# Optimization experiments

Measured on AMD Instinct MI355X. Metric: run time of the kernel, lower is better.

Reference implementation:

```python
import jax, jax.numpy as jnp
import numpy as np

SOFTCLAMP = 50.0
CAUSAL_BLOCK = 256      # causal_block_size (tokens per time block)
NUM_SPECIAL = 8         # num_special_tokens
SPECIAL_SEQ = 2048      # block_size_per_special (defaults to kv seq len)
ROPE_BASE = 10000.0


def setup_inputs() -> dict:
    key = jax.random.key(0)
    kq, kk, kv = jax.random.split(key, 3)
    b, h, hk, s, d = 2, 16, 4, 2048, 64
    q = jax.random.normal(kq, (b, h, s, d), dtype=jnp.float32)
    k = jax.random.normal(kk, (b, hk, s, d), dtype=jnp.float32)
    v = jax.random.normal(kv, (b, hk, s, d), dtype=jnp.float32)
    # standard 1D rotary angles: [seq, dim_head]
    inv_freq = 1.0 / (ROPE_BASE ** (jnp.arange(0, d, 2, dtype=jnp.float32) / d))
    freqs = jnp.arange(s, dtype=jnp.float32)[:, None] * inv_freq[None, :]  # [s, d/2]
    rotations = jnp.concatenate((freqs, freqs), axis=-1)                   # [s, d]
    return {"q": q, "k": k, "v": v, "rotations": rotations}


def _apply_rotations(rotations, t):
    # t: [b, h, s, d]; rotations: [s, d] (broadcast over batch/heads)
    x1, x2 = jnp.split(t, 2, axis=-1)
    rotated_half = jnp.concatenate((-x2, x1), axis=-1)
    return t * jnp.cos(rotations) + rotated_half * jnp.sin(rotations)


def _forward(q, k, v, rotations):
    b, h, i, d = q.shape
    hk, j = k.shape[1], k.shape[2]
    scale = d ** -0.5
    q = _apply_rotations(rotations[:i], q)
    k = _apply_rotations(rotations[:j], k)
    g = h // hk  # GQA groups
    qg = q.reshape(b, hk, g, i, d)
    sim = jnp.einsum('bhgid,bhjd->bhgij', qg, k) * scale
    # softclamp score mod
    sim = jnp.tanh(sim / SOFTCLAMP) * SOFTCLAMP
    # special-token mask (faithful to source: compares raw q/k indices)
    qi = jnp.arange(i)[:, None]
    kj = jnp.arange(j)[None, :]
    special_start = SPECIAL_SEQ - NUM_SPECIAL
    q_is_special = qi >= special_start
    k_is_special = kj >= special_start
    special_mask = ~(~q_is_special & k_is_special)  # non-special q cannot see special k
    # block-causal mask: allowed when query block >= key block
    causal_allow = (qi // CAUSAL_BLOCK) >= (kj // CAUSAL_BLOCK)
    allow = special_mask & causal_allow  # [i, j], broadcasts over b,h,g
    mask_value = -jnp.finfo(sim.dtype).max
    sim = jnp.where(allow, sim, mask_value)
    attn = jax.nn.softmax(sim, axis=-1)
    out = jnp.einsum('bhgij,bhjd->bhgid', attn, v)
    return out.reshape(b, h, i, d)


def reference(q, k, v, rotations):
    return _forward(q, k, v, rotations)
```

## Files before the change

kernel.cpp:

```cpp
#include <hip/hip_runtime.h>
#include <stdint.h>

typedef unsigned short u16;
typedef short s16x8 __attribute__((ext_vector_type(8)));
typedef float f32x4 __attribute__((ext_vector_type(4)));

#define SQ 2048
#define DH 64
#define BM 64
#define BN 64
#define STR 72
#define SPECIAL_START 2040
#define NBH 32
#define NKV 8
#define NQT 32
#define NITEMS (NBH * NQT)
#define ATTN_GRID 896
#define K1F  0.18033688011112043f
#define KPAF 4.9244826e-9f
#define KPBF -6.406040185576019e-5f
#define KEF  36.067376022224085f

union U8 { s16x8 v; short e[8]; };
union F4 { f32x4 v; float e[4]; };

__device__ __forceinline__ u16 f2bf(float x) {
    uint32_t u = __float_as_uint(x);
    return (u16)((u + 0x7fffu + ((u >> 16) & 1u)) >> 16);
}
__device__ __forceinline__ uint32_t pkbf(float a, float b) {
    uint32_t r;
    asm("v_cvt_pk_bf16_f32 %0, %1, %2" : "=v"(r) : "v"(a), "v"(b));
    return r;
}
__device__ __forceinline__ float exp2hw(float x) {
    float r; asm("v_exp_f32 %0, %1" : "=v"(r) : "v"(x)); return r;
}
__device__ __forceinline__ float2 fsincos(float ang) {
    float r = ang * 0.15915494309189535f;
    r -= floorf(r);
    float s, c;
    asm("v_sin_f32 %0, %1" : "=v"(s) : "v"(r));
    asm("v_cos_f32 %0, %1" : "=v"(c) : "v"(r));
    return make_float2(s, c);
}

#define VTILES (NKV * 32)
#define RQ (NBH * SQ)
#define RK (NKV * SQ)
#define QKBLK ((RQ + RK) / 32)
__global__ __launch_bounds__(256)
void prep_kernel(const float* __restrict__ qg, const float* __restrict__ kg,
                 const float* __restrict__ vg, const float* __restrict__ rotg,
                 u16* __restrict__ qp, u16* __restrict__ kp, u16* __restrict__ vp,
                 uint32_t* __restrict__ cnt, int init_cnt)
{
    const int tid = threadIdx.x;
    if (init_cnt && blockIdx.x == 0 && tid == 0) *cnt = 0u;
    if (blockIdx.x < VTILES) {
        __shared__ short Vls[64 * STR];
        const int tile = blockIdx.x;
        const float* src = vg + ((size_t)(tile >> 5) * SQ + (size_t)(tile & 31) * 64) * DH;
        {
            int kv = tid >> 2, c0 = (tid & 3) * 16;
            const float* s4 = src + (size_t)kv * DH + c0;
            float4 f0 = *(const float4*)(s4);
            float4 f1 = *(const float4*)(s4 + 4);
            float4 f2 = *(const float4*)(s4 + 8);
            float4 f3 = *(const float4*)(s4 + 12);
            uint4 w0 = make_uint4(pkbf(f0.x, f0.y), pkbf(f0.z, f0.w),
                                  pkbf(f1.x, f1.y), pkbf(f1.z, f1.w));
            uint4 w1 = make_uint4(pkbf(f2.x, f2.y), pkbf(f2.z, f2.w),
                                  pkbf(f3.x, f3.y), pkbf(f3.z, f3.w));
            *(uint4*)&Vls[kv * STR + c0]     = w0;
            *(uint4*)&Vls[kv * STR + c0 + 8] = w1;
        }
        __syncthreads();
        {
            int d = tid >> 2, c0 = (tid & 3) * 16;
            U8 o0, o1;
#pragma unroll
            for (int j = 0; j < 16; j++)
                (j < 8 ? o0 : o1).e[j & 7] = Vls[(c0 + j) * STR + d];
            u16* dst = vp + (((size_t)tile * 64 + d) << 6) + c0;
            *(s16x8*)dst       = o0.v;
            *(s16x8*)(dst + 8) = o1.v;
        }
    } else {
        int bx = blockIdx.x - VTILES;
        int r8 = tid >> 3, c0 = (tid & 7) * 4;
        int R = bx * 32 + r8;
        const int isQ = (R < RQ);
        const int r = isQ ? R : R - RQ;
        const int s = r & (SQ - 1);
        const float* src = (isQ ? qg : kg) + (size_t)r * DH;
        u16*         dst = (isQ ? qp : kp) + (size_t)r * DH;
        float4 a  = *(const float4*)(src + c0);
        float4 b  = *(const float4*)(src + c0 + 32);
        float4 rv = *(const float4*)(rotg + (size_t)s * DH + c0);
        float2 s0 = fsincos(rv.x), s1 = fsincos(rv.y),
               s2 = fsincos(rv.z), s3 = fsincos(rv.w);
        float lo0 = a.x * s0.y - b.x * s0.x, hi0 = b.x * s0.y + a.x * s0.x;
        float lo1 = a.y * s1.y - b.y * s1.x, hi1 = b.y * s1.y + a.y * s1.x;
        float lo2 = a.z * s2.y - b.z * s2.x, hi2 = b.z * s2.y + a.z * s2.x;
        float lo3 = a.w * s3.y - b.w * s3.x, hi3 = b.w * s3.y + a.w * s3.x;
        *(uint2*)(dst + c0)      = make_uint2(pkbf(lo0, lo1), pkbf(lo2, lo3));
        *(uint2*)(dst + c0 + 32) = make_uint2(pkbf(hi0, hi1), pkbf(hi2, hi3));
    }
}

__global__ __launch_bounds__(256, 4)
void attn_kernel(const float* __restrict__ qg, const float* __restrict__ kg,
                 const float* __restrict__ vg, const float* __restrict__ rotg,
                 int mode,
                 const u16* __restrict__ qp, const u16* __restrict__ kp,
                 const u16* __restrict__ vp, uint32_t* __restrict__ cnt,
                 float* __restrict__ outg)
{
    const int tid = threadIdx.x;
    const int wv = tid >> 6, lane = tid & 63;
    const int l15 = lane & 15, quad = lane >> 4;
    const int r4 = tid >> 2, c16 = (tid & 3) * 16;
    const int swl = (l15 & 7) << 3;
    const int swr = (r4 & 7) << 3;

    __shared__ __align__(16) short QPs[BM * 64];
    __shared__ __align__(16) short Ks[2][BN * 64];
    __shared__ __align__(16) short Vt[2][DH * 64];
    volatile int* s_w = (volatile int*)&Ks[1][BN * 64 - 2];

    int done = 0;
    for (;;) {
        int qt, bh;
        if (mode == 2) {
            __syncthreads();
            if (tid == 0) *s_w = (int)atomicAdd(cnt, 1u);
            __syncthreads();
            const int w = *s_w;
            if (w >= NITEMS) break;
            qt = (NQT - 1) - (w >> 5);
            bh = w & (NBH - 1);
        } else {
            if (done) break;
            done = 1;
            const int x = blockIdx.x;
            qt = (x & 1) ? (31 - (x >> 1)) : (x >> 1);
            bh = blockIdx.y;
        }

        const int bb = bh >> 4, hh = bh & 15;
        const int bkv = bb * 4 + (hh >> 2);
        const int qs = qt * BM;
        const size_t qbase  = ((size_t)bh * SQ + qs) * DH;
        const size_t kvbase = ((size_t)bkv * SQ) * DH;
        const int nkt = (qt / 4 + 1) * 4;
        const int qglob = qs + wv * 16 + l15;

        s16x8 kpr0, kpr1, vpr0, vpr1;
        auto pref = [&](int kt) {
            const u16* srck = kp + kvbase + (size_t)(kt * BN + r4) * DH + c16;
            kpr0 = *(const s16x8*)srck;
            kpr1 = *(const s16x8*)(srck + 8);
            const u16* srcv = vp + (((size_t)(bkv * 32 + kt) * 64 + r4) << 6) + c16;
            vpr0 = *(const s16x8*)srcv;
            vpr1 = *(const s16x8*)(srcv + 8);
        };
        if (mode) pref(0);

        if (mode) {
            const u16* src = qp + qbase + (size_t)r4 * DH + c16;
            *(s16x8*)&QPs[r4 * 64 + (c16 ^ swr)]       = *(const s16x8*)src;
            *(s16x8*)&QPs[r4 * 64 + ((c16 + 8) ^ swr)] = *(const s16x8*)(src + 8);
        } else {
            int rr = tid >> 2, c0 = (tid & 3) * 8;
            int srow = qs + rr;
            const float* gq = qg + qbase + (size_t)rr * DH;
            float a[8], b[8];
            *(float4*)&a[0] = *(const float4*)(gq + c0);
            *(float4*)&a[4] = *(const float4*)(gq + c0 + 4);
            *(float4*)&b[0] = *(const float4*)(gq + c0 + 32);
            *(float4*)&b[4] = *(const float4*)(gq + c0 + 36);
            U8 o0, o1;
#pragma unroll
            for (int j = 0; j < 8; j++) {
                float cs, sn;
                sincosf(rotg[(size_t)srow * DH + ((c0 + j) & 31)], &sn, &cs);
                o0.e[j] = (short)f2bf(a[j] * cs - b[j] * sn);
                o1.e[j] = (short)f2bf(b[j] * cs + a[j] * sn);
            }
            int sw2 = (rr & 7) << 3;
            *(s16x8*)&QPs[rr * 64 + (c0 ^ sw2)]        = o0.v;
            *(s16x8*)&QPs[rr * 64 + ((c0 + 32) ^ sw2)] = o1.v;
        }
        __syncthreads();

        s16x8 qf[2];
#pragma unroll
        for (int ks = 0; ks < 2; ks++)
            qf[ks] = *(const s16x8*)&QPs[(wv * 16 + l15) * 64 + ((ks * 32 + quad * 8) ^ swl)];

        F4 oa[4];
#pragma unroll
        for (int mb = 0; mb < 4; mb++) oa[mb].v = (f32x4){0.f, 0.f, 0.f, 0.f};
        float lsum = 0.f;

#pragma unroll 2
        for (int kt = 0; kt < nkt; kt++) {
            const int cb = kt & 1;
            if (mode) {
                *(s16x8*)&Ks[cb][r4 * 64 + (c16 ^ swr)]       = kpr0;
                *(s16x8*)&Ks[cb][r4 * 64 + ((c16 + 8) ^ swr)] = kpr1;
                *(s16x8*)&Vt[cb][r4 * 64 + (c16 ^ swr)]       = vpr0;
                *(s16x8*)&Vt[cb][r4 * 64 + ((c16 + 8) ^ swr)] = vpr1;
                if (kt + 1 < nkt) pref(kt + 1);
            } else {
                {
                    int rr = tid >> 2, c0 = (tid & 3) * 8;
                    int srow = kt * BN + rr;
                    const float* gk = kg + kvbase + (size_t)srow * DH;
                    float a[8], b[8];
                    *(float4*)&a[0] = *(const float4*)(gk + c0);
                    *(float4*)&a[4] = *(const float4*)(gk + c0 + 4);
                    *(float4*)&b[0] = *(const float4*)(gk + c0 + 32);
                    *(float4*)&b[4] = *(const float4*)(gk + c0 + 36);
                    U8 o0, o1;
#pragma unroll
                    for (int j = 0; j < 8; j++) {
                        float cs, sn;
                        sincosf(rotg[(size_t)srow * DH + ((c0 + j) & 31)], &sn, &cs);
                        o0.e[j] = (short)f2bf(a[j] * cs - b[j] * sn);
                        o1.e[j] = (short)f2bf(b[j] * cs + a[j] * sn);
                    }
                    int sw2 = (rr & 7) << 3;
                    *(s16x8*)&Ks[cb][rr * 64 + (c0 ^ sw2)]        = o0.v;
                    *(s16x8*)&Ks[cb][rr * 64 + ((c0 + 32) ^ sw2)] = o1.v;
                }
                {
                    int rr = tid >> 2, c0 = (tid & 3) * 16;
                    const float* gv = vg + kvbase + (size_t)(kt * BN + rr) * DH;
                    float vv[16];
#pragma unroll
                    for (int t = 0; t < 4; t++)
                        *(float4*)&vv[t * 4] = *(const float4*)(gv + c0 + t * 4);
#pragma unroll
                    for (int j = 0; j < 16; j++) {
                        int d = c0 + j;
                        Vt[cb][d * 64 + (rr ^ ((d & 7) << 3))] = (short)f2bf(vv[j]);
                    }
                }
            }
            __syncthreads();

            F4 sa[4];
#pragma unroll
            for (int mb = 0; mb < 4; mb++) sa[mb].v = (f32x4){0.f, 0.f, 0.f, 0.f};
            __builtin_amdgcn_s_setprio(1);
#pragma unroll
            for (int ks = 0; ks < 2; ks++) {
#pragma unroll
                for (int mb = 0; mb < 4; mb++) {
                    s16x8 kf = *(const s16x8*)&Ks[cb][(mb * 16 + l15) * 64 + ((ks * 32 + quad * 8) ^ swl)];
                    sa[mb].v = __builtin_amdgcn_mfma_f32_16x16x32_bf16(kf, qf[ks], sa[mb].v, 0, 0, 0);
                }
            }
            __builtin_amdgcn_s_setprio(0);

            F4 pa[4];
#pragma unroll
            for (int mb = 0; mb < 4; mb++)
#pragma unroll
                for (int c = 0; c < 4; c++) {
                    float t  = sa[mb].e[c] * K1F;
                    float w2 = t * t;
                    float poly = fmaf(w2, fmaf(w2, KPAF, KPBF), 1.0f);
                    pa[mb].e[c] = exp2hw(fmaf(t, poly, -KEF));
                }
            if (kt == 31 && qglob < SPECIAL_START) {
#pragma unroll
                for (int mb = 0; mb < 4; mb++)
#pragma unroll
                    for (int c = 0; c < 4; c++) {
                        int kvglob = kt * BN + mb * 16 + quad * 4 + c;
                        if (kvglob >= SPECIAL_START) pa[mb].e[c] = 0.f;
                    }
            }
            short* prow = &QPs[(wv * 16 + l15) * 64];
#pragma unroll
            for (int mb = 0; mb < 4; mb++) {
                lsum += pa[mb].e[0] + pa[mb].e[1] + pa[mb].e[2] + pa[mb].e[3];
                uint2 pw = make_uint2(pkbf(pa[mb].e[0], pa[mb].e[1]),
                                      pkbf(pa[mb].e[2], pa[mb].e[3]));
                *(uint2*)&prow[(mb * 16 + quad * 4) ^ swl] = pw;
            }

            __builtin_amdgcn_s_setprio(1);
#pragma unroll
            for (int ks = 0; ks < 2; ks++) {
                s16x8 pf = *(const s16x8*)&prow[(ks * 32 + quad * 8) ^ swl];
#pragma unroll
                for (int mb = 0; mb < 4; mb++) {
                    s16x8 vf = *(const s16x8*)&Vt[cb][(mb * 16 + l15) * 64 + ((ks * 32 + quad * 8) ^ swl)];
                    oa[mb].v = __builtin_amdgcn_mfma_f32_16x16x32_bf16(vf, pf, oa[mb].v, 0, 0, 0);
                }
            }
            __builtin_amdgcn_s_setprio(0);
        }

        lsum += __shfl_xor(lsum, 16, 64);
        lsum += __shfl_xor(lsum, 32, 64);

        float rl = 1.0f / lsum;
        int qrow = qs + wv * 16 + l15;
        float* orow = outg + ((size_t)bh * SQ + qrow) * DH;
#pragma unroll
        for (int mb = 0; mb < 4; mb++) {
            int d0 = mb * 16 + quad * 4;
            *(float4*)(orow + d0) = make_float4(oa[mb].e[0] * rl, oa[mb].e[1] * rl,
                                                oa[mb].e[2] * rl, oa[mb].e[3] * rl);
        }
    }
}

extern "C" void kernel_launch(void* const* d_in, const int* in_sizes, int n_in,
                              void* d_out, int out_size, void* d_ws, size_t ws_size,
                              hipStream_t stream) {
    const float* q   = (const float*)d_in[0];
    const float* k   = (const float*)d_in[1];
    const float* v   = (const float*)d_in[2];
    const float* rot = (const float*)d_in[3];
    float* out = (float*)d_out;

    char* w = (char*)d_ws;
    const size_t q_bytes = (size_t)NBH * SQ * DH * sizeof(u16);
    const size_t k_bytes = (size_t)NKV * SQ * DH * sizeof(u16);
    const size_t v_bytes = k_bytes;
    const size_t base = q_bytes + k_bytes + v_bytes;
    u16* qp = (u16*)w;
    u16* kp = (u16*)(w + q_bytes);
    u16* vp = (u16*)(w + q_bytes + k_bytes);
    uint32_t* cnt = (uint32_t*)(w + base);

    int mode = 0;
    if (ws_size >= base + sizeof(uint32_t)) mode = 2;
    else if (ws_size >= base) mode = 1;

    if (mode)
        hipLaunchKernelGGL(prep_kernel, dim3(VTILES + QKBLK), dim3(256), 0, stream,
                           q, k, v, rot, qp, kp, vp, cnt, (mode == 2) ? 1 : 0);

    if (mode == 2)
        hipLaunchKernelGGL(attn_kernel, dim3(ATTN_GRID), dim3(256), 0, stream,
                           q, k, v, rot, mode, qp, kp, vp, cnt, out);
    else
        hipLaunchKernelGGL(attn_kernel, dim3(32, NBH), dim3(256), 0, stream,
                           q, k, v, rot, mode, qp, kp, vp, cnt, out);
}
```

Before: 149.1 us.

## Read K/V MFMA fragments directly from global memory and fuse Q rotary into attention

The attention kernel stops staging K and V tiles in LDS. Each wave loads its MFMA fragments straight from the bf16 prepped buffers in global memory, which drops the per-tile LDS writes and block barriers. Q rotary and bf16 conversion now happen inside the attention kernel, so prep only converts K and V, and work items are reordered so heads sharing a KV group run adjacently to improve L2 reuse. In exchange, every wave re-reads the K/V data from L2 rather than sharing one LDS copy, and occupancy is raised to 6 blocks per CU.

```diff
diff --git a/kernel.cpp b/kernel.cpp
--- a/kernel.cpp
+++ b/kernel.cpp
@@ -46,17 +46,16 @@
 }
 
 #define VTILES (NKV * 32)
-#define RQ (NBH * SQ)
 #define RK (NKV * SQ)
-#define QKBLK ((RQ + RK) / 32)
+#define KBLK (RK / 32)
 __global__ __launch_bounds__(256)
-void prep_kernel(const float* __restrict__ qg, const float* __restrict__ kg,
-                 const float* __restrict__ vg, const float* __restrict__ rotg,
-                 u16* __restrict__ qp, u16* __restrict__ kp, u16* __restrict__ vp,
-                 uint32_t* __restrict__ cnt, int init_cnt)
+void prep_kernel(const float* __restrict__ kg, const float* __restrict__ vg,
+                 const float* __restrict__ rotg,
+                 u16* __restrict__ kp, u16* __restrict__ vp,
+                 uint32_t* __restrict__ cnt)
 {
     const int tid = threadIdx.x;
-    if (init_cnt && blockIdx.x == 0 && tid == 0) *cnt = 0u;
+    if (blockIdx.x == 0 && tid == 0) *cnt = 0u;
     if (blockIdx.x < VTILES) {
         __shared__ short Vls[64 * STR];
         const int tile = blockIdx.x;
@@ -89,12 +88,10 @@
     } else {
         int bx = blockIdx.x - VTILES;
         int r8 = tid >> 3, c0 = (tid & 7) * 4;
-        int R = bx * 32 + r8;
-        const int isQ = (R < RQ);
-        const int r = isQ ? R : R - RQ;
+        int r = bx * 32 + r8;
         const int s = r & (SQ - 1);
-        const float* src = (isQ ? qg : kg) + (size_t)r * DH;
-        u16*         dst = (isQ ? qp : kp) + (size_t)r * DH;
+        const float* src = kg + (size_t)r * DH;
+        u16*         dst = kp + (size_t)r * DH;
         float4 a  = *(const float4*)(src + c0);
         float4 b  = *(const float4*)(src + c0 + 32);
         float4 rv = *(const float4*)(rotg + (size_t)s * DH + c0);
@@ -109,90 +106,57 @@
     }
 }
 
-__global__ __launch_bounds__(256, 4)
-void attn_kernel(const float* __restrict__ qg, const float* __restrict__ kg,
-                 const float* __restrict__ vg, const float* __restrict__ rotg,
-                 int mode,
-                 const u16* __restrict__ qp, const u16* __restrict__ kp,
-                 const u16* __restrict__ vp, uint32_t* __restrict__ cnt,
-                 float* __restrict__ outg)
+__global__ __launch_bounds__(256, 6)
+void attn_fast(const float* __restrict__ qg, const float* __restrict__ rotg,
+               const u16* __restrict__ kp, const u16* __restrict__ vp,
+               uint32_t* __restrict__ cnt, float* __restrict__ outg)
 {
     const int tid = threadIdx.x;
     const int wv = tid >> 6, lane = tid & 63;
     const int l15 = lane & 15, quad = lane >> 4;
-    const int r4 = tid >> 2, c16 = (tid & 3) * 16;
     const int swl = (l15 & 7) << 3;
-    const int swr = (r4 & 7) << 3;
 
     __shared__ __align__(16) short QPs[BM * 64];
-    __shared__ __align__(16) short Ks[2][BN * 64];
-    __shared__ __align__(16) short Vt[2][DH * 64];
-    volatile int* s_w = (volatile int*)&Ks[1][BN * 64 - 2];
-
-    int done = 0;
+    __shared__ int s_w;
+
     for (;;) {
-        int qt, bh;
-        if (mode == 2) {
-            __syncthreads();
-            if (tid == 0) *s_w = (int)atomicAdd(cnt, 1u);
-            __syncthreads();
-            const int w = *s_w;
-            if (w >= NITEMS) break;
-            qt = (NQT - 1) - (w >> 5);
-            bh = w & (NBH - 1);
-        } else {
-            if (done) break;
-            done = 1;
-            const int x = blockIdx.x;
-            qt = (x & 1) ? (31 - (x >> 1)) : (x >> 1);
-            bh = blockIdx.y;
-        }
-
-        const int bb = bh >> 4, hh = bh & 15;
-        const int bkv = bb * 4 + (hh >> 2);
+        __syncthreads();
+        if (tid == 0) s_w = (int)atomicAdd(cnt, 1u);
+        __syncthreads();
+        const int w = s_w;
+        if (w >= NITEMS) break;
+        const int qt = (NQT - 1) - (w >> 5);
+        const int u  = w & 31, bkv = u >> 2;
+        const int bh = ((bkv >> 2) << 4) | ((bkv & 3) << 2) | (u & 3);
         const int qs = qt * BM;
-        const size_t qbase  = ((size_t)bh * SQ + qs) * DH;
-        const size_t kvbase = ((size_t)bkv * SQ) * DH;
         const int nkt = (qt / 4 + 1) * 4;
         const int qglob = qs + wv * 16 + l15;
 
-        s16x8 kpr0, kpr1, vpr0, vpr1;
-        auto pref = [&](int kt) {
-            const u16* srck = kp + kvbase + (size_t)(kt * BN + r4) * DH + c16;
-            kpr0 = *(const s16x8*)srck;
-            kpr1 = *(const s16x8*)(srck + 8);
-            const u16* srcv = vp + (((size_t)(bkv * 32 + kt) * 64 + r4) << 6) + c16;
-            vpr0 = *(const s16x8*)srcv;
-            vpr1 = *(const s16x8*)(srcv + 8);
-        };
-        if (mode) pref(0);
-
-        if (mode) {
-            const u16* src = qp + qbase + (size_t)r4 * DH + c16;
-            *(s16x8*)&QPs[r4 * 64 + (c16 ^ swr)]       = *(const s16x8*)src;
-            *(s16x8*)&QPs[r4 * 64 + ((c16 + 8) ^ swr)] = *(const s16x8*)(src + 8);
-        } else {
-            int rr = tid >> 2, c0 = (tid & 3) * 8;
-            int srow = qs + rr;
-            const float* gq = qg + qbase + (size_t)rr * DH;
+        {
+            const int rr = tid >> 2, c0 = (tid & 3) * 8;
+            const int srow = qs + rr;
+            const float* gq = qg + ((size_t)bh * SQ + srow) * DH;
             float a[8], b[8];
             *(float4*)&a[0] = *(const float4*)(gq + c0);
             *(float4*)&a[4] = *(const float4*)(gq + c0 + 4);
             *(float4*)&b[0] = *(const float4*)(gq + c0 + 32);
             *(float4*)&b[4] = *(const float4*)(gq + c0 + 36);
-            U8 o0, o1;
+            const float* rrow = rotg + (size_t)srow * DH + c0;
+            float lo[8], hi[8];
 #pragma unroll
             for (int j = 0; j < 8; j++) {
-                float cs, sn;
-                sincosf(rotg[(size_t)srow * DH + ((c0 + j) & 31)], &sn, &cs);
-                o0.e[j] = (short)f2bf(a[j] * cs - b[j] * sn);
-                o1.e[j] = (short)f2bf(b[j] * cs + a[j] * sn);
-            }
-            int sw2 = (rr & 7) << 3;
-            *(s16x8*)&QPs[rr * 64 + (c0 ^ sw2)]        = o0.v;
-            *(s16x8*)&QPs[rr * 64 + ((c0 + 32) ^ sw2)] = o1.v;
-        }
-        __syncthreads();
+                float2 sc = fsincos(rrow[j]);
+                lo[j] = a[j] * sc.y - b[j] * sc.x;
+                hi[j] = b[j] * sc.y + a[j] * sc.x;
+            }
+            const int sw2 = (rr & 7) << 3;
+            uint4 w0 = make_uint4(pkbf(lo[0], lo[1]), pkbf(lo[2], lo[3]),
+                                  pkbf(lo[4], lo[5]), pkbf(lo[6], lo[7]));
+            uint4 w1 = make_uint4(pkbf(hi[0], hi[1]), pkbf(hi[2], hi[3]),
+                                  pkbf(hi[4], hi[5]), pkbf(hi[6], hi[7]));
+            *(uint4*)&QPs[rr * 64 + (c0 ^ sw2)]          = w0;
+            *(uint4*)&QPs[rr * 64 + ((c0 + 32) ^ sw2)]   = w1;
+        }
 
         s16x8 qf[2];
 #pragma unroll
@@ -204,65 +168,25 @@
         for (int mb = 0; mb < 4; mb++) oa[mb].v = (f32x4){0.f, 0.f, 0.f, 0.f};
         float lsum = 0.f;
 
+        const u16* kbl = kp + (size_t)bkv * (SQ * DH) + l15 * 64 + quad * 8;
+        const u16* vbl = vp + (size_t)bkv * (32 * 64 * 64) + l15 * 64 + quad * 8;
+        short* prow = &QPs[(wv * 16 + l15) * 64];
+
 #pragma unroll 2
         for (int kt = 0; kt < nkt; kt++) {
-            const int cb = kt & 1;
-            if (mode) {
-                *(s16x8*)&Ks[cb][r4 * 64 + (c16 ^ swr)]       = kpr0;
-                *(s16x8*)&Ks[cb][r4 * 64 + ((c16 + 8) ^ swr)] = kpr1;
-                *(s16x8*)&Vt[cb][r4 * 64 + (c16 ^ swr)]       = vpr0;
-                *(s16x8*)&Vt[cb][r4 * 64 + ((c16 + 8) ^ swr)] = vpr1;
-                if (kt + 1 < nkt) pref(kt + 1);
-            } else {
-                {
-                    int rr = tid >> 2, c0 = (tid & 3) * 8;
-                    int srow = kt * BN + rr;
-                    const float* gk = kg + kvbase + (size_t)srow * DH;
-                    float a[8], b[8];
-                    *(float4*)&a[0] = *(const float4*)(gk + c0);
-                    *(float4*)&a[4] = *(const float4*)(gk + c0 + 4);
-                    *(float4*)&b[0] = *(const float4*)(gk + c0 + 32);
-                    *(float4*)&b[4] = *(const float4*)(gk + c0 + 36);
-                    U8 o0, o1;
-#pragma unroll
-                    for (int j = 0; j < 8; j++) {
-                        float cs, sn;
-                        sincosf(rotg[(size_t)srow * DH + ((c0 + j) & 31)], &sn, &cs);
-                        o0.e[j] = (short)f2bf(a[j] * cs - b[j] * sn);
-                        o1.e[j] = (short)f2bf(b[j] * cs + a[j] * sn);
-                    }
-                    int sw2 = (rr & 7) << 3;
-                    *(s16x8*)&Ks[cb][rr * 64 + (c0 ^ sw2)]        = o0.v;
-                    *(s16x8*)&Ks[cb][rr * 64 + ((c0 + 32) ^ sw2)] = o1.v;
+            const u16* kt_k = kbl + (size_t)kt * 4096;
+            const u16* kt_v = vbl + (size_t)kt * 4096;
+
+            F4 sa[4];
+            __builtin_amdgcn_s_setprio(1);
+#pragma unroll
+            for (int ks = 0; ks < 2; ks++)
+#pragma unroll
+                for (int mb = 0; mb < 4; mb++) {
+                    s16x8 kf = *(const s16x8*)(kt_k + mb * 1024 + ks * 32);
+                    sa[mb].v = __builtin_amdgcn_mfma_f32_16x16x32_bf16(
+                        kf, qf[ks], ks ? sa[mb].v : (f32x4){0.f, 0.f, 0.f, 0.f}, 0, 0, 0);
                 }
-                {
-                    int rr = tid >> 2, c0 = (tid & 3) * 16;
-                    const float* gv = vg + kvbase + (size_t)(kt * BN + rr) * DH;
-                    float vv[16];
-#pragma unroll
-                    for (int t = 0; t < 4; t++)
-                        *(float4*)&vv[t * 4] = *(const float4*)(gv + c0 + t * 4);
-#pragma unroll
-                    for (int j = 0; j < 16; j++) {
-                        int d = c0 + j;
-                        Vt[cb][d * 64 + (rr ^ ((d & 7) << 3))] = (short)f2bf(vv[j]);
-                    }
-                }
-            }
-            __syncthreads();
-
-            F4 sa[4];
-#pragma unroll
-            for (int mb = 0; mb < 4; mb++) sa[mb].v = (f32x4){0.f, 0.f, 0.f, 0.f};
-            __builtin_amdgcn_s_setprio(1);
-#pragma unroll
-            for (int ks = 0; ks < 2; ks++) {
-#pragma unroll
-                for (int mb = 0; mb < 4; mb++) {
-                    s16x8 kf = *(const s16x8*)&Ks[cb][(mb * 16 + l15) * 64 + ((ks * 32 + quad * 8) ^ swl)];
-                    sa[mb].v = __builtin_amdgcn_mfma_f32_16x16x32_bf16(kf, qf[ks], sa[mb].v, 0, 0, 0);
-                }
-            }
             __builtin_amdgcn_s_setprio(0);
 
             F4 pa[4];
@@ -284,10 +208,9 @@
                         if (kvglob >= SPECIAL_START) pa[mb].e[c] = 0.f;
                     }
             }
-            short* prow = &QPs[(wv * 16 + l15) * 64];
 #pragma unroll
             for (int mb = 0; mb < 4; mb++) {
-                lsum += pa[mb].e[0] + pa[mb].e[1] + pa[mb].e[2] + pa[mb].e[3];
+                lsum += (pa[mb].e[0] + pa[mb].e[1]) + (pa[mb].e[2] + pa[mb].e[3]);
                 uint2 pw = make_uint2(pkbf(pa[mb].e[0], pa[mb].e[1]),
                                       pkbf(pa[mb].e[2], pa[mb].e[3]));
                 *(uint2*)&prow[(mb * 16 + quad * 4) ^ swl] = pw;
@@ -299,7 +222,7 @@
                 s16x8 pf = *(const s16x8*)&prow[(ks * 32 + quad * 8) ^ swl];
 #pragma unroll
                 for (int mb = 0; mb < 4; mb++) {
-                    s16x8 vf = *(const s16x8*)&Vt[cb][(mb * 16 + l15) * 64 + ((ks * 32 + quad * 8) ^ swl)];
+                    s16x8 vf = *(const s16x8*)(kt_v + mb * 1024 + ks * 32);
                     oa[mb].v = __builtin_amdgcn_mfma_f32_16x16x32_bf16(vf, pf, oa[mb].v, 0, 0, 0);
                 }
             }
@@ -318,6 +241,164 @@
             *(float4*)(orow + d0) = make_float4(oa[mb].e[0] * rl, oa[mb].e[1] * rl,
                                                 oa[mb].e[2] * rl, oa[mb].e[3] * rl);
         }
+    }
+}
+
+__global__ __launch_bounds__(256, 4)
+void attn_fallback(const float* __restrict__ qg, const float* __restrict__ kg,
+                   const float* __restrict__ vg, const float* __restrict__ rotg,
+                   float* __restrict__ outg)
+{
+    const int x  = blockIdx.x;
+    const int qt = (x & 1) ? (31 - (x >> 1)) : (x >> 1);
+    const int bh = blockIdx.y;
+    const int bb = bh >> 4, hh = bh & 15;
+    const int bkv = bb * 4 + (hh >> 2);
+    const int qs = qt * BM;
+
+    const int tid = threadIdx.x;
+    const int wv = tid >> 6, lane = tid & 63;
+    const int l15 = lane & 15, quad = lane >> 4;
+    const int swl = (l15 & 7) << 3;
+
+    __shared__ __align__(16) short QPs[BM * 64];
+    __shared__ __align__(16) short Ks[2][BN * 64];
+    __shared__ __align__(16) short Vt[2][DH * 64];
+
+    const size_t kvbase = ((size_t)bkv * SQ) * DH;
+    const int nkt = (qt / 4 + 1) * 4;
+    const int qglob = qs + wv * 16 + l15;
+
+    {
+        int rr = tid >> 2, c0 = (tid & 3) * 8;
+        int srow = qs + rr;
+        const float* gq = qg + ((size_t)bh * SQ + srow) * DH;
+        float a[8], b[8];
+        *(float4*)&a[0] = *(const float4*)(gq + c0);
+        *(float4*)&a[4] = *(const float4*)(gq + c0 + 4);
+        *(float4*)&b[0] = *(const float4*)(gq + c0 + 32);
+        *(float4*)&b[4] = *(const float4*)(gq + c0 + 36);
+        U8 o0, o1;
+#pragma unroll
+        for (int j = 0; j < 8; j++) {
+            float2 sc = fsincos(rotg[(size_t)srow * DH + c0 + j]);
+            o0.e[j] = (short)f2bf(a[j] * sc.y - b[j] * sc.x);
+            o1.e[j] = (short)f2bf(b[j] * sc.y + a[j] * sc.x);
+        }
+        int sw2 = (rr & 7) << 3;
+        *(s16x8*)&QPs[rr * 64 + (c0 ^ sw2)]        = o0.v;
+        *(s16x8*)&QPs[rr * 64 + ((c0 + 32) ^ sw2)] = o1.v;
+    }
+    __syncthreads();
+
+    s16x8 qf[2];
+#pragma unroll
+    for (int ks = 0; ks < 2; ks++)
+        qf[ks] = *(const s16x8*)&QPs[(wv * 16 + l15) * 64 + ((ks * 32 + quad * 8) ^ swl)];
+
+    F4 oa[4];
+#pragma unroll
+    for (int mb = 0; mb < 4; mb++) oa[mb].v = (f32x4){0.f, 0.f, 0.f, 0.f};
+    float lsum = 0.f;
+
+    for (int kt = 0; kt < nkt; kt++) {
+        const int cb = kt & 1;
+        {
+            int rr = tid >> 2, c0 = (tid & 3) * 8;
+            int srow = kt * BN + rr;
+            const float* gk = kg + kvbase + (size_t)srow * DH;
+            float a[8], b[8];
+            *(float4*)&a[0] = *(const float4*)(gk + c0);
+            *(float4*)&a[4] = *(const float4*)(gk + c0 + 4);
+            *(float4*)&b[0] = *(const float4*)(gk + c0 + 32);
+            *(float4*)&b[4] = *(const float4*)(gk + c0 + 36);
+            U8 o0, o1;
+#pragma unroll
+            for (int j = 0; j < 8; j++) {
+                float2 sc = fsincos(rotg[(size_t)(srow & (SQ - 1)) * DH + c0 + j]);
+                o0.e[j] = (short)f2bf(a[j] * sc.y - b[j] * sc.x);
+                o1.e[j] = (short)f2bf(b[j] * sc.y + a[j] * sc.x);
+            }
+            int sw2 = (rr & 7) << 3;
+            *(s16x8*)&Ks[cb][rr * 64 + (c0 ^ sw2)]        = o0.v;
+            *(s16x8*)&Ks[cb][rr * 64 + ((c0 + 32) ^ sw2)] = o1.v;
+        }
+        {
+            int rr = tid >> 2, c0 = (tid & 3) * 16;
+            const float* gv = vg + kvbase + (size_t)(kt * BN + rr) * DH;
+            float vv[16];
+#pragma unroll
+            for (int t = 0; t < 4; t++)
+                *(float4*)&vv[t * 4] = *(const float4*)(gv + c0 + t * 4);
+#pragma unroll
+            for (int j = 0; j < 16; j++) {
+                int d = c0 + j;
+                Vt[cb][d * 64 + (rr ^ ((d & 7) << 3))] = (short)f2bf(vv[j]);
+            }
+        }
+        __syncthreads();
+
+        F4 sa[4];
+#pragma unroll
+        for (int mb = 0; mb < 4; mb++) sa[mb].v = (f32x4){0.f, 0.f, 0.f, 0.f};
+#pragma unroll
+        for (int ks = 0; ks < 2; ks++)
+#pragma unroll
+            for (int mb = 0; mb < 4; mb++) {
+                s16x8 kf = *(const s16x8*)&Ks[cb][(mb * 16 + l15) * 64 + ((ks * 32 + quad * 8) ^ swl)];
+                sa[mb].v = __builtin_amdgcn_mfma_f32_16x16x32_bf16(kf, qf[ks], sa[mb].v, 0, 0, 0);
+            }
+
+        F4 pa[4];
+#pragma unroll
+        for (int mb = 0; mb < 4; mb++)
+#pragma unroll
+            for (int c = 0; c < 4; c++) {
+                float t  = sa[mb].e[c] * K1F;
+                float w2 = t * t;
+                float poly = fmaf(w2, fmaf(w2, KPAF, KPBF), 1.0f);
+                pa[mb].e[c] = exp2hw(fmaf(t, poly, -KEF));
+            }
+        if (kt == 31 && qglob < SPECIAL_START) {
+#pragma unroll
+            for (int mb = 0; mb < 4; mb++)
+#pragma unroll
+                for (int c = 0; c < 4; c++) {
+                    int kvglob = kt * BN + mb * 16 + quad * 4 + c;
+                    if (kvglob >= SPECIAL_START) pa[mb].e[c] = 0.f;
+                }
+        }
+        short* prow = &QPs[(wv * 16 + l15) * 64];
+#pragma unroll
+        for (int mb = 0; mb < 4; mb++) {
+            lsum += (pa[mb].e[0] + pa[mb].e[1]) + (pa[mb].e[2] + pa[mb].e[3]);
+            uint2 pw = make_uint2(pkbf(pa[mb].e[0], pa[mb].e[1]),
+                                  pkbf(pa[mb].e[2], pa[mb].e[3]));
+            *(uint2*)&prow[(mb * 16 + quad * 4) ^ swl] = pw;
+        }
+#pragma unroll
+        for (int ks = 0; ks < 2; ks++) {
+            s16x8 pf = *(const s16x8*)&prow[(ks * 32 + quad * 8) ^ swl];
+#pragma unroll
+            for (int mb = 0; mb < 4; mb++) {
+                s16x8 vf = *(const s16x8*)&Vt[cb][(mb * 16 + l15) * 64 + ((ks * 32 + quad * 8) ^ swl)];
+                oa[mb].v = __builtin_amdgcn_mfma_f32_16x16x32_bf16(vf, pf, oa[mb].v, 0, 0, 0);
+            }
+        }
+        __syncthreads();
+    }
+
+    lsum += __shfl_xor(lsum, 16, 64);
+    lsum += __shfl_xor(lsum, 32, 64);
+
+    float rl = 1.0f / lsum;
+    int qrow = qs + wv * 16 + l15;
+    float* orow = outg + ((size_t)bh * SQ + qrow) * DH;
+#pragma unroll
+    for (int mb = 0; mb < 4; mb++) {
+        int d0 = mb * 16 + quad * 4;
+        *(float4*)(orow + d0) = make_float4(oa[mb].e[0] * rl, oa[mb].e[1] * rl,
+                                            oa[mb].e[2] * rl, oa[mb].e[3] * rl);
     }
 }
 
@@ -331,27 +412,19 @@
     float* out = (float*)d_out;
 
     char* w = (char*)d_ws;
-    const size_t q_bytes = (size_t)NBH * SQ * DH * sizeof(u16);
     const size_t k_bytes = (size_t)NKV * SQ * DH * sizeof(u16);
     const size_t v_bytes = k_bytes;
-    const size_t base = q_bytes + k_bytes + v_bytes;
-    u16* qp = (u16*)w;
-    u16* kp = (u16*)(w + q_bytes);
-    u16* vp = (u16*)(w + q_bytes + k_bytes);
-    uint32_t* cnt = (uint32_t*)(w + base);
-
-    int mode = 0;
-    if (ws_size >= base + sizeof(uint32_t)) mode = 2;
-    else if (ws_size >= base) mode = 1;
-
-    if (mode)
-        hipLaunchKernelGGL(prep_kernel, dim3(VTILES + QKBLK), dim3(256), 0, stream,
-                           q, k, v, rot, qp, kp, vp, cnt, (mode == 2) ? 1 : 0);
-
-    if (mode == 2)
-        hipLaunchKernelGGL(attn_kernel, dim3(ATTN_GRID), dim3(256), 0, stream,
-                           q, k, v, rot, mode, qp, kp, vp, cnt, out);
-    else
-        hipLaunchKernelGGL(attn_kernel, dim3(32, NBH), dim3(256), 0, stream,
-                           q, k, v, rot, mode, qp, kp, vp, cnt, out);
-}
+    u16* kp = (u16*)w;
+    u16* vp = (u16*)(w + k_bytes);
+    uint32_t* cnt = (uint32_t*)(w + k_bytes + v_bytes);
+
+    if (ws_size >= k_bytes + v_bytes + sizeof(uint32_t)) {
+        hipLaunchKernelGGL(prep_kernel, dim3(VTILES + KBLK), dim3(256), 0, stream,
+                           k, v, rot, kp, vp, cnt);
+        hipLaunchKernelGGL(attn_fast, dim3(ATTN_GRID), dim3(256), 0, stream,
+                           q, rot, kp, vp, cnt, out);
+    } else {
+        hipLaunchKernelGGL(attn_fallback, dim3(32, NBH), dim3(256), 0, stream,
+                           q, k, v, rot, out);
+    }
+}
```

Result: slower. 249.8 us (+67.6%).
